# Kernel optimization log

Hardware: AMD Instinct MI355X
Metric: run time of the kernel (lower is better)

Reference implementation:

```python
import jax, jax.numpy as jnp
import numpy as np

IN_FEATURES = 4096
OUT_FEATURES = 11008
GROUP_SIZE = 128
NUM_GROUPS = IN_FEATURES // GROUP_SIZE  # 32
BATCH, SEQ = 4, 2048


def setup_inputs() -> dict:
    key = jax.random.key(0)
    k_in, k_w, k_s, k_b = jax.random.split(key, 4)
    inp = jax.random.normal(k_in, (BATCH, SEQ, IN_FEATURES), dtype=jnp.float32)
    # 4-bit symmetric codes in [-8, 8)
    weight = jax.random.randint(k_w, (OUT_FEATURES, NUM_GROUPS, GROUP_SIZE), -8, 8, dtype=jnp.int32)
    # small positive per-group scales, as produced by quantization calibration
    scales = jax.random.uniform(k_s, (OUT_FEATURES, NUM_GROUPS), dtype=jnp.float32) * 0.02 + 1e-4
    bias = jax.random.normal(k_b, (OUT_FEATURES,), dtype=jnp.float32)
    return {"input": inp, "weight": weight, "scales": scales, "bias": bias}


def reference(input, weight, scales, bias):
    # Fused dequant-matmul: symmetric weight-only quantization.
    # weight: [O, G, gs] int codes; scales: [O, G] per-group scale.
    O, G, gs = weight.shape
    W = weight.astype(jnp.float32) * scales[:, :, None]   # [O, G, gs] dequantized
    W = W.reshape(O, G * gs)                               # [O, in_features]
    out = jnp.einsum('bsi,oi->bso', input, W)              # [B, S, O]
    return out + bias
```

## Files before the change

### kernel.cpp

```cpp
#include <hip/hip_runtime.h>
#include <hip/hip_bf16.h>
#include <cstdint>

#define M_DIM 8192
#define K_DIM 4096
#define N_DIM 11008
#define NGROUPS 32

typedef __attribute__((ext_vector_type(4))) float f32x4;
typedef __attribute__((ext_vector_type(4))) int i32x4;
typedef __attribute__((ext_vector_type(8))) __bf16 bf16x8;

__device__ __forceinline__ unsigned int f2bf(float f) {
  unsigned int u = __builtin_bit_cast(unsigned int, f);
  return (u + 0x7FFFu + ((u >> 16) & 1u)) >> 16;
}
__device__ __forceinline__ unsigned int pk2(float lo, float hi) {
  return f2bf(lo) | (f2bf(hi) << 16);
}

__global__ __launch_bounds__(256) void quantA_kernel(const float* __restrict__ in,
                                                     char* __restrict__ outA,
                                                     float* __restrict__ sA) {
  const int row = blockIdx.x * 4 + (threadIdx.x >> 6);
  const int lane = threadIdx.x & 63;
  const float* p = in + (size_t)row * K_DIM;
  float mx = 0.f;
#pragma unroll
  for (int e = 0; e < 16; ++e) {
    float4 v = *(const float4*)(p + e * 256 + lane * 4);
    mx = fmaxf(mx, fmaxf(fmaxf(fabsf(v.x), fabsf(v.y)), fmaxf(fabsf(v.z), fabsf(v.w))));
  }
#pragma unroll
  for (int off = 32; off; off >>= 1) mx = fmaxf(mx, __shfl_xor(mx, off));
  mx = fmaxf(mx, 1e-30f);
  const float rq = 127.f / mx;
  if (lane == 0) sA[row] = mx / 127.f;
  char* op = outA + (size_t)row * K_DIM;
#pragma unroll
  for (int e = 0; e < 16; ++e) {
    float4 v = *(const float4*)(p + e * 256 + lane * 4);
    unsigned pk = ((unsigned)((int)rintf(v.x * rq)) & 0xFFu)
                | (((unsigned)((int)rintf(v.y * rq)) & 0xFFu) << 8)
                | (((unsigned)((int)rintf(v.z * rq)) & 0xFFu) << 16)
                | (((unsigned)((int)rintf(v.w * rq)) & 0xFFu) << 24);
    *(unsigned*)(op + e * 256 + lane * 4) = pk;
  }
}

__global__ __launch_bounds__(256) void quantW_kernel(const int* __restrict__ wc,
                                                     const float* __restrict__ sc,
                                                     char* __restrict__ outB,
                                                     float* __restrict__ sW) {
  const int col = blockIdx.x * 4 + (threadIdx.x >> 6);
  const int lane = threadIdx.x & 63;
  const int4* p = (const int4*)(wc + (size_t)col * K_DIM);
  const float* scp = sc + col * NGROUPS;
  float mx = 0.f;
#pragma unroll
  for (int e = 0; e < 16; ++e) {
    int4 c = p[e * 64 + lane];
    float s = scp[e * 2 + (lane >> 5)];
    float m = fmaxf(fmaxf(fabsf((float)c.x), fabsf((float)c.y)),
                    fmaxf(fabsf((float)c.z), fabsf((float)c.w)));
    mx = fmaxf(mx, m * s);
  }
#pragma unroll
  for (int off = 32; off; off >>= 1) mx = fmaxf(mx, __shfl_xor(mx, off));
  mx = fmaxf(mx, 1e-30f);
  const float rq = 127.f / mx;
  if (lane == 0) sW[col] = mx / 127.f;
  char* op = outB + (size_t)col * K_DIM;
#pragma unroll
  for (int e = 0; e < 16; ++e) {
    int4 c = p[e * 64 + lane];
    float s = scp[e * 2 + (lane >> 5)] * rq;
    unsigned pk = ((unsigned)((int)rintf((float)c.x * s)) & 0xFFu)
                | (((unsigned)((int)rintf((float)c.y * s)) & 0xFFu) << 8)
                | (((unsigned)((int)rintf((float)c.z * s)) & 0xFFu) << 16)
                | (((unsigned)((int)rintf((float)c.w * s)) & 0xFFu) << 24);
    *(unsigned*)(op + e * 256 + lane * 4) = pk;
  }
}

__device__ __forceinline__ void gload16(const void* g, void* l) {
  __builtin_amdgcn_global_load_lds((const __attribute__((address_space(1))) void*)g,
                                   (__attribute__((address_space(3))) void*)l,
                                   16, 0, 0);
}

#define BM 256
#define BN 256
#define BKB 64
#define NKT (K_DIM / BKB)
#define TILES_M (M_DIM / BM)
#define TILES_N (N_DIM / BN)
#define NB2 (TILES_M * TILES_N)
#define TSZ (BM * BKB)

#define VMCNT_(n) asm volatile("s_waitcnt vmcnt(" #n ")" ::: "memory")
#define VMCNT(n) VMCNT_(n)
#define BAR() __builtin_amdgcn_s_barrier()

__global__ __launch_bounds__(512, 2) void gemmq_kernel(
    const char* __restrict__ A,
    const char* __restrict__ B,
    const float* __restrict__ sA,
    const float* __restrict__ sW,
    const float* __restrict__ bias,
    float* __restrict__ out) {
  __shared__ __align__(16) char lA[2][TSZ];
  __shared__ __align__(16) char lB[2][TSZ];

  const int t = threadIdx.x;
  const int bid = blockIdx.x;
  const int wg = (bid & 7) * (NB2 / 8) + (bid >> 3);
  const int m0 = (wg / TILES_N) * BM;
  const int n0 = (wg % TILES_N) * BN;

  const int w = t >> 6;
  const int lane = t & 63;
  const int wm = w >> 2;
  const int wn = w & 3;

  const int r0 = w * 32 + (lane >> 2);
  const int r1 = r0 + 16;
  const int pgs = lane & 3;
  const size_t aoff0 = (size_t)(m0 + r0) * K_DIM + (unsigned)(pgs ^ ((r0 >> 1) & 3)) * 16;
  const size_t aoff1 = (size_t)(m0 + r1) * K_DIM + (unsigned)(pgs ^ ((r1 >> 1) & 3)) * 16;
  const size_t boff0 = (size_t)(n0 + r0) * K_DIM + (unsigned)(pgs ^ ((r0 >> 1) & 3)) * 16;
  const size_t boff1 = (size_t)(n0 + r1) * K_DIM + (unsigned)(pgs ^ ((r1 >> 1) & 3)) * 16;
  const int ld0 = w * 2048;
  const int ld1 = w * 2048 + 1024;

  i32x4 acc[8][4];
#pragma unroll
  for (int i = 0; i < 8; ++i)
#pragma unroll
    for (int j = 0; j < 4; ++j) {
      i32x4 z = {0, 0, 0, 0};
      acc[i][j] = z;
    }

#define STAGE(buf, kt)                                                        \
  do {                                                                        \
    gload16(A + aoff0 + (size_t)(kt) * BKB, &lA[buf][ld0]);                   \
    gload16(A + aoff1 + (size_t)(kt) * BKB, &lA[buf][ld1]);                   \
    gload16(B + boff0 + (size_t)(kt) * BKB, &lB[buf][ld0]);                   \
    gload16(B + boff1 + (size_t)(kt) * BKB, &lB[buf][ld1]);                   \
  } while (0)

#define TILE_CORE(CB)                                                         \
  i32x4 af[8], bq[4];                                                         \
  _Pragma("unroll") for (int i = 0; i < 8; ++i) {                             \
    const int row = wm * 128 + i * 16 + (lane & 15);                          \
    const int pg = (lane >> 4) ^ ((row >> 1) & 3);                            \
    af[i] = *(const i32x4*)&lA[CB][row * 64 + pg * 16];                       \
  }                                                                           \
  _Pragma("unroll") for (int j = 0; j < 4; ++j) {                             \
    const int row = wn * 64 + j * 16 + (lane & 15);                           \
    const int pg = (lane >> 4) ^ ((row >> 1) & 3);                            \
    bq[j] = *(const i32x4*)&lB[CB][row * 64 + pg * 16];                       \
  }

#define TILE_MMA()                                                            \
  __builtin_amdgcn_s_setprio(1);                                              \
  _Pragma("unroll") for (int i = 0; i < 8; ++i)                               \
  _Pragma("unroll") for (int j = 0; j < 4; ++j)                               \
    acc[i][j] = __builtin_amdgcn_mfma_i32_16x16x64_i8(af[i], bq[j],           \
                                                      acc[i][j], 0, 0, 0);    \
  __builtin_amdgcn_s_setprio(0);

#define TILE(CB, NB_, KT)                                                     \
  {                                                                           \
    TILE_CORE(CB)                                                             \
    STAGE(NB_, (KT) + 1);                                                     \
    TILE_MMA()                                                                \
    VMCNT(0);                                                                 \
    BAR();                                                                    \
  }

  STAGE(0, 0);
  VMCNT(0);
  BAR();

  for (int it = 0; it < 31; ++it) {
    TILE(0, 1, 2 * it)
    TILE(1, 0, 2 * it + 1)
  }
  TILE(0, 1, 62)
  {
    TILE_CORE(1)
    TILE_MMA()
  }

  const int colb = n0 + wn * 64 + (lane & 15);
  const int rowb = m0 + wm * 128 + ((lane >> 4) << 2);
  float sar[8][4];
#pragma unroll
  for (int ai = 0; ai < 8; ++ai)
#pragma unroll
    for (int r = 0; r < 4; ++r)
      sar[ai][r] = sA[rowb + ai * 16 + r];
#pragma unroll
  for (int j = 0; j < 4; ++j) {
    const int col = colb + j * 16;
    const float sc2 = sW[col];
    const float bv = bias[col];
#pragma unroll
    for (int ai = 0; ai < 8; ++ai) {
      const int row = rowb + ai * 16;
#pragma unroll
      for (int r = 0; r < 4; ++r)
        out[(size_t)(row + r) * N_DIM + col] =
            (float)acc[ai][j][r] * sar[ai][r] * sc2 + bv;
    }
  }
#undef STAGE
#undef TILE_CORE
#undef TILE_MMA
#undef TILE
}

#define FBM 128
#define FBN 128
#define FBK 64
#define FNT_N 86
#define FNT_M 64
#define FNB (FNT_N * FNT_M)

__global__ __launch_bounds__(256, 2) void gemm_fb_kernel(
    const float* __restrict__ Ain, const int* __restrict__ Wcodes,
    const float* __restrict__ scales, const float* __restrict__ bias,
    float* __restrict__ out) {
  __shared__ unsigned short lsA[FBM * FBK];
  __shared__ unsigned short lsB[FBN * FBK];

  const int t = threadIdx.x;
  const int bid = blockIdx.x;
  const int wg = (bid & 7) * (FNB / 8) + (bid >> 3);
  const int m0 = (wg / FNT_N) * FBM;
  const int n0 = (wg % FNT_N) * FBN;

  const int w = t >> 6;
  const int lane = t & 63;
  const int wm = w >> 1, wn = w & 1;
  const int srow = t >> 3;
  const int sp = t & 7;
  const int skc = sp ^ (srow & 7);

  f32x4 acc[4][4];
#pragma unroll
  for (int i = 0; i < 4; ++i)
#pragma unroll
    for (int j = 0; j < 4; ++j) {
      f32x4 z = {0.f, 0.f, 0.f, 0.f};
      acc[i][j] = z;
    }

  for (int kt = 0; kt < K_DIM / FBK; ++kt) {
    const int kg = kt * FBK + skc * 8;
#pragma unroll
    for (int c = 0; c < 4; ++c) {
      const int arow = m0 + c * 32 + srow;
      const float* ap = Ain + (size_t)arow * K_DIM + kg;
      float4 a0 = *(const float4*)ap;
      float4 a1 = *(const float4*)(ap + 4);
      uint4 va;
      va.x = pk2(a0.x, a0.y); va.y = pk2(a0.z, a0.w);
      va.z = pk2(a1.x, a1.y); va.w = pk2(a1.z, a1.w);
      *(uint4*)&lsA[(c * 32 + srow) * FBK + sp * 8] = va;

      const int nrow = n0 + c * 32 + srow;
      const float s = scales[nrow * NGROUPS + (kg >> 7)];
      const int4* wp = (const int4*)(Wcodes + (size_t)nrow * K_DIM + kg);
      int4 c0 = wp[0], c1 = wp[1];
      uint4 vb;
      vb.x = pk2((float)c0.x * s, (float)c0.y * s);
      vb.y = pk2((float)c0.z * s, (float)c0.w * s);
      vb.z = pk2((float)c1.x * s, (float)c1.y * s);
      vb.w = pk2((float)c1.z * s, (float)c1.w * s);
      *(uint4*)&lsB[(c * 32 + srow) * FBK + sp * 8] = vb;
    }
    __syncthreads();
#pragma unroll
    for (int kk = 0; kk < 2; ++kk) {
      bf16x8 af[4], bfr[4];
#pragma unroll
      for (int i = 0; i < 4; ++i) {
        const int row = wm * 64 + i * 16 + (lane & 15);
        const int pg = (kk * 4 + (lane >> 4)) ^ (row & 7);
        af[i] = *(const bf16x8*)&lsA[row * FBK + pg * 8];
      }
#pragma unroll
      for (int j = 0; j < 4; ++j) {
        const int row = wn * 64 + j * 16 + (lane & 15);
        const int pg = (kk * 4 + (lane >> 4)) ^ (row & 7);
        bfr[j] = *(const bf16x8*)&lsB[row * FBK + pg * 8];
      }
#pragma unroll
      for (int i = 0; i < 4; ++i)
#pragma unroll
        for (int j = 0; j < 4; ++j)
          acc[i][j] = __builtin_amdgcn_mfma_f32_16x16x32_bf16(af[i], bfr[j], acc[i][j], 0, 0, 0);
    }
    __syncthreads();
  }

  const int colb = n0 + wn * 64 + (lane & 15);
  const int rowb = m0 + wm * 64 + ((lane >> 4) << 2);
#pragma unroll
  for (int j = 0; j < 4; ++j) {
    const int col = colb + j * 16;
    const float bv = bias[col];
#pragma unroll
    for (int i = 0; i < 4; ++i) {
      const int row = rowb + i * 16;
#pragma unroll
      for (int r = 0; r < 4; ++r)
        out[(size_t)(row + r) * N_DIM + col] = acc[i][j][r] + bv;
    }
  }
}

extern "C" void kernel_launch(void* const* d_in, const int* in_sizes, int n_in,
                              void* d_out, int out_size, void* d_ws, size_t ws_size,
                              hipStream_t stream) {
  const float* Ain = (const float*)d_in[0];
  const int* Wc = (const int*)d_in[1];
  const float* sc = (const float*)d_in[2];
  const float* bias = (const float*)d_in[3];
  float* out = (float*)d_out;

  const size_t offW = (size_t)M_DIM * K_DIM;
  const size_t offSA = offW + (size_t)N_DIM * K_DIM;
  const size_t offSW = offSA + (size_t)M_DIM * 4;
  const size_t need = offSW + (size_t)N_DIM * 4;

  if (ws_size >= need) {
    char* wsA = (char*)d_ws;
    char* wsB = (char*)d_ws + offW;
    float* sA = (float*)((char*)d_ws + offSA);
    float* sW = (float*)((char*)d_ws + offSW);
    quantA_kernel<<<M_DIM / 4, 256, 0, stream>>>(Ain, wsA, sA);
    quantW_kernel<<<N_DIM / 4, 256, 0, stream>>>(Wc, sc, wsB, sW);
    gemmq_kernel<<<NB2, 512, 0, stream>>>(wsA, wsB, sA, sW, bias, out);
  } else {
    gemm_fb_kernel<<<FNB, 256, 0, stream>>>(Ain, Wc, sc, bias, out);
  }
}
```

Baseline: 566.5 us.

## Halve N tile, triple-buffer LDS loads, and raise launch-bounds occupancy

Shrinks the int8 GEMM block tile from 256x256 to 256x128 and rearranges the 8 waves as 4x2 with 64x64 sub-tiles each. LDS staging goes from double to triple buffering, and the wait becomes vmcnt(3) so one tile's loads stay in flight across the barrier. Launch bounds request 4 blocks per CU to hide latency with more resident work. In exchange, the smaller tile lowers arithmetic intensity and doubles A-operand traffic. The 72 KB of LDS per block plus the tighter register budget may prevent the requested occupancy or cause register spills.

```diff
diff --git a/kernel.cpp b/kernel.cpp
--- a/kernel.cpp
+++ b/kernel.cpp
@@ -90,27 +90,28 @@
 }
 
 #define BM 256
-#define BN 256
+#define BN 128
 #define BKB 64
 #define NKT (K_DIM / BKB)
 #define TILES_M (M_DIM / BM)
 #define TILES_N (N_DIM / BN)
 #define NB2 (TILES_M * TILES_N)
-#define TSZ (BM * BKB)
+#define TSZA (BM * BKB)
+#define TSZB (BN * BKB)
 
 #define VMCNT_(n) asm volatile("s_waitcnt vmcnt(" #n ")" ::: "memory")
 #define VMCNT(n) VMCNT_(n)
 #define BAR() __builtin_amdgcn_s_barrier()
 
-__global__ __launch_bounds__(512, 2) void gemmq_kernel(
+__global__ __launch_bounds__(512, 4) void gemmq_kernel(
     const char* __restrict__ A,
     const char* __restrict__ B,
     const float* __restrict__ sA,
     const float* __restrict__ sW,
     const float* __restrict__ bias,
     float* __restrict__ out) {
-  __shared__ __align__(16) char lA[2][TSZ];
-  __shared__ __align__(16) char lB[2][TSZ];
+  __shared__ __align__(16) char lA[3][TSZA];
+  __shared__ __align__(16) char lB[3][TSZB];
 
   const int t = threadIdx.x;
   const int bid = blockIdx.x;
@@ -120,22 +121,23 @@
 
   const int w = t >> 6;
   const int lane = t & 63;
-  const int wm = w >> 2;
-  const int wn = w & 3;
-
-  const int r0 = w * 32 + (lane >> 2);
-  const int r1 = r0 + 16;
+  const int wm = w >> 1;
+  const int wn = w & 1;
+
+  const int ra0 = w * 32 + (lane >> 2);
+  const int ra1 = ra0 + 16;
+  const int rb = w * 16 + (lane >> 2);
   const int pgs = lane & 3;
-  const size_t aoff0 = (size_t)(m0 + r0) * K_DIM + (unsigned)(pgs ^ ((r0 >> 1) & 3)) * 16;
-  const size_t aoff1 = (size_t)(m0 + r1) * K_DIM + (unsigned)(pgs ^ ((r1 >> 1) & 3)) * 16;
-  const size_t boff0 = (size_t)(n0 + r0) * K_DIM + (unsigned)(pgs ^ ((r0 >> 1) & 3)) * 16;
-  const size_t boff1 = (size_t)(n0 + r1) * K_DIM + (unsigned)(pgs ^ ((r1 >> 1) & 3)) * 16;
-  const int ld0 = w * 2048;
-  const int ld1 = w * 2048 + 1024;
-
-  i32x4 acc[8][4];
-#pragma unroll
-  for (int i = 0; i < 8; ++i)
+  const size_t aoff0 = (size_t)(m0 + ra0) * K_DIM + (unsigned)(pgs ^ ((ra0 >> 1) & 3)) * 16;
+  const size_t aoff1 = (size_t)(m0 + ra1) * K_DIM + (unsigned)(pgs ^ ((ra1 >> 1) & 3)) * 16;
+  const size_t boff = (size_t)(n0 + rb) * K_DIM + (unsigned)(pgs ^ ((rb >> 1) & 3)) * 16;
+  const int ldA0 = w * 2048;
+  const int ldA1 = w * 2048 + 1024;
+  const int ldB = w * 1024;
+
+  i32x4 acc[4][4];
+#pragma unroll
+  for (int i = 0; i < 4; ++i)
 #pragma unroll
     for (int j = 0; j < 4; ++j) {
       i32x4 z = {0, 0, 0, 0};
@@ -144,16 +146,15 @@
 
 #define STAGE(buf, kt)                                                        \
   do {                                                                        \
-    gload16(A + aoff0 + (size_t)(kt) * BKB, &lA[buf][ld0]);                   \
-    gload16(A + aoff1 + (size_t)(kt) * BKB, &lA[buf][ld1]);                   \
-    gload16(B + boff0 + (size_t)(kt) * BKB, &lB[buf][ld0]);                   \
-    gload16(B + boff1 + (size_t)(kt) * BKB, &lB[buf][ld1]);                   \
+    gload16(A + aoff0 + (size_t)(kt) * BKB, &lA[buf][ldA0]);                  \
+    gload16(A + aoff1 + (size_t)(kt) * BKB, &lA[buf][ldA1]);                  \
+    gload16(B + boff + (size_t)(kt) * BKB, &lB[buf][ldB]);                    \
   } while (0)
 
 #define TILE_CORE(CB)                                                         \
-  i32x4 af[8], bq[4];                                                         \
-  _Pragma("unroll") for (int i = 0; i < 8; ++i) {                             \
-    const int row = wm * 128 + i * 16 + (lane & 15);                          \
+  i32x4 af[4], bq[4];                                                         \
+  _Pragma("unroll") for (int i = 0; i < 4; ++i) {                             \
+    const int row = wm * 64 + i * 16 + (lane & 15);                           \
     const int pg = (lane >> 4) ^ ((row >> 1) & 3);                            \
     af[i] = *(const i32x4*)&lA[CB][row * 64 + pg * 16];                       \
   }                                                                           \
@@ -165,40 +166,50 @@
 
 #define TILE_MMA()                                                            \
   __builtin_amdgcn_s_setprio(1);                                              \
-  _Pragma("unroll") for (int i = 0; i < 8; ++i)                               \
+  _Pragma("unroll") for (int i = 0; i < 4; ++i)                               \
   _Pragma("unroll") for (int j = 0; j < 4; ++j)                               \
     acc[i][j] = __builtin_amdgcn_mfma_i32_16x16x64_i8(af[i], bq[j],           \
                                                       acc[i][j], 0, 0, 0);    \
   __builtin_amdgcn_s_setprio(0);
 
-#define TILE(CB, NB_, KT)                                                     \
+#define TILE(CB, SB, KT2)                                                     \
   {                                                                           \
     TILE_CORE(CB)                                                             \
-    STAGE(NB_, (KT) + 1);                                                     \
+    STAGE(SB, KT2);                                                           \
     TILE_MMA()                                                                \
-    VMCNT(0);                                                                 \
+    VMCNT(3);                                                                 \
     BAR();                                                                    \
   }
 
   STAGE(0, 0);
-  VMCNT(0);
+  STAGE(1, 1);
+  VMCNT(3);
   BAR();
 
-  for (int it = 0; it < 31; ++it) {
-    TILE(0, 1, 2 * it)
-    TILE(1, 0, 2 * it + 1)
-  }
-  TILE(0, 1, 62)
+  for (int it = 0; it < 20; ++it) {
+    const int k = 3 * it;
+    TILE(0, 2, k + 2)
+    TILE(1, 0, k + 3)
+    TILE(2, 1, k + 4)
+  }
+  TILE(0, 2, 62)
+  TILE(1, 0, 63)
   {
-    TILE_CORE(1)
+    TILE_CORE(2)
     TILE_MMA()
+    VMCNT(0);
+    BAR();
+  }
+  {
+    TILE_CORE(0)
+    TILE_MMA()
   }
 
   const int colb = n0 + wn * 64 + (lane & 15);
-  const int rowb = m0 + wm * 128 + ((lane >> 4) << 2);
-  float sar[8][4];
-#pragma unroll
-  for (int ai = 0; ai < 8; ++ai)
+  const int rowb = m0 + wm * 64 + ((lane >> 4) << 2);
+  float sar[4][4];
+#pragma unroll
+  for (int ai = 0; ai < 4; ++ai)
 #pragma unroll
     for (int r = 0; r < 4; ++r)
       sar[ai][r] = sA[rowb + ai * 16 + r];
@@ -208,7 +219,7 @@
     const float sc2 = sW[col];
     const float bv = bias[col];
 #pragma unroll
-    for (int ai = 0; ai < 8; ++ai) {
+    for (int ai = 0; ai < 4; ++ai) {
       const int row = rowb + ai * 16;
 #pragma unroll
       for (int r = 0; r < 4; ++r)
```

Result: faster. 519.2 us (-8.3%).
